# Kernel optimization log

Hardware: AMD Instinct MI355X
Metric: run time of the kernel (lower is better)

## Reference

```python
import jax, jax.numpy as jnp
import numpy as np

SUB_ARRAY_RATIO = 0.5
CENTER = False
EPS = 1e-8


def setup_inputs() -> dict:
    key = jax.random.key(0)
    X = jax.random.normal(key, (256, 8, 16384), dtype=jnp.float32)
    return {"X": X}


def reference(X) -> jnp.ndarray:
    # X: (N, M, T) real -> cast to complex64 (matches torch _ensure_complex)
    N, M, T = X.shape
    Xc = X - X.mean(axis=-1, keepdims=True) if CENTER else X
    Xc = Xc.astype(jnp.complex64)

    S = max(2, min(int(M * SUB_ARRAY_RATIO) + 1, M))  # sub_array_size
    J = M - S + 1                                      # number_of_sub_arrays

    # Full sample covariance C = X X^H / T, shape (N, M, M).
    # The per-window covariance R_j is just the SxS diagonal block of C at offset j,
    # so the forward-smoothed covariance is the mean of J shifted diagonal blocks.
    C = jnp.einsum("nmt,nkt->nmk", Xc, jnp.conj(Xc)) / T

    win = jnp.arange(J)[:, None] + jnp.arange(S)[None, :]  # (J, S) window row indices
    # Gather all J diagonal blocks: (N, J, S, S), then average over windows.
    R = C[:, win[:, :, None], win[:, None, :]].mean(axis=1)  # (N, S, S)

    rows, cols = jnp.triu_indices(S)
    tri = R[:, rows, cols]                                   # (N, S*(S+1)/2) complex
    feat = jnp.concatenate([tri.real, tri.imag], axis=1).astype(jnp.float32)

    mean = feat.mean(axis=1, keepdims=True)
    std = feat.std(axis=1, keepdims=True)  # correction=0, matches torch
    return (feat - mean) / (std + EPS)
```

## Files before the change

kernel.cpp:

```cpp
#include <hip/hip_runtime.h>
#include <math.h>

#define TLEN 16384
#define MROW 8
#define NPAIR 36
#define NTHREADS 512
#define EPSV 1e-8f

__global__ __launch_bounds__(NTHREADS)
void ssf_kernel(const float* __restrict__ X, float* __restrict__ out) {
    const int n   = blockIdx.x;
    const int tid = threadIdx.x;
    const float4* Xv = reinterpret_cast<const float4*>(X + (size_t)n * MROW * TLEN);
    const int TV = TLEN / 4;

    float acc[NPAIR];
#pragma unroll
    for (int p = 0; p < NPAIR; ++p) acc[p] = 0.f;

    for (int it = tid; it < TV; it += NTHREADS) {
        float4 x[MROW];
#pragma unroll
        for (int m = 0; m < MROW; ++m) x[m] = Xv[m * TV + it];
        const float* xv = reinterpret_cast<const float*>(x);
#pragma unroll
        for (int e = 0; e < 4; ++e) {
            int p = 0;
#pragma unroll
            for (int m = 0; m < MROW; ++m) {
                const float vm = xv[m * 4 + e];
#pragma unroll
                for (int k = m; k < MROW; ++k) {
                    acc[p++] += vm * xv[k * 4 + e];
                }
            }
        }
    }

#pragma unroll
    for (int p = 0; p < NPAIR; ++p) {
        float v = acc[p];
#pragma unroll
        for (int off = 32; off > 0; off >>= 1) v += __shfl_down(v, off, 64);
        acc[p] = v;
    }

    __shared__ float partial[NTHREADS / 64][NPAIR];
    __shared__ float Cm[MROW][MROW];
    const int wave = tid >> 6;
    const int lane = tid & 63;
    if (lane == 0) {
#pragma unroll
        for (int p = 0; p < NPAIR; ++p) partial[wave][p] = acc[p];
    }
    __syncthreads();

    if (tid < NPAIR) {
        float s = 0.f;
#pragma unroll
        for (int w = 0; w < NTHREADS / 64; ++w) s += partial[w][tid];
        s *= (1.0f / (float)TLEN);
        int p = tid, m = 0;
        while (p >= (MROW - m)) { p -= (MROW - m); ++m; }
        const int k = m + p;
        Cm[m][k] = s;
        Cm[k][m] = s;
    }
    __syncthreads();

    if (tid == 0) {
        const int rows[15] = {0,0,0,0,0, 1,1,1,1, 2,2,2, 3,3, 4};
        const int cols[15] = {0,1,2,3,4, 1,2,3,4, 2,3,4, 3,4, 4};
        float tri[15];
        float sum = 0.f;
#pragma unroll
        for (int i = 0; i < 15; ++i) {
            float r = 0.f;
#pragma unroll
            for (int j = 0; j < 4; ++j) r += Cm[j + rows[i]][j + cols[i]];
            r *= 0.25f;
            tri[i] = r;
            sum += r;
        }
        const float mean = sum * (1.0f / 30.0f);
        float var = 0.f;
#pragma unroll
        for (int i = 0; i < 15; ++i) { const float d = tri[i] - mean; var += d * d; }
        var += 15.0f * mean * mean;
        var *= (1.0f / 30.0f);
        const float inv = 1.0f / (sqrtf(var) + EPSV);

        float* o = out + (size_t)n * 30;
#pragma unroll
        for (int i = 0; i < 15; ++i) o[i] = (tri[i] - mean) * inv;
        const float zi = -mean * inv;
#pragma unroll
        for (int i = 0; i < 15; ++i) o[15 + i] = zi;
    }
}

extern "C" void kernel_launch(void* const* d_in, const int* in_sizes, int n_in,
                              void* d_out, int out_size, void* d_ws, size_t ws_size,
                              hipStream_t stream) {
    const float* X = (const float*)d_in[0];
    float* out = (float*)d_out;
    ssf_kernel<<<256, NTHREADS, 0, stream>>>(X, out);
}
```

Before: 188.4 us.

## Split time axis across blocks with two-pass reduction and prune unused pairs

Splits each sample's time axis into 8 chunks handled by separate 256-thread blocks, writing per-chunk partial covariance sums to workspace, then a second small kernel reduces them and computes features. It also only accumulates covariance entries within distance 4 of the diagonal, since only those are used by the smoothed blocks. This aims to fill the GPU with many more blocks to hide memory latency, at the cost of an extra launch and workspace traffic.

```diff
diff --git a/kernel.cpp b/kernel.cpp
--- a/kernel.cpp
+++ b/kernel.cpp
@@ -3,22 +3,29 @@
 
 #define TLEN 16384
 #define MROW 8
-#define NPAIR 36
-#define NTHREADS 512
+#define NPAIR 30
+#define NCHUNK 8
+#define NT1 256
 #define EPSV 1e-8f
 
-__global__ __launch_bounds__(NTHREADS)
-void ssf_kernel(const float* __restrict__ X, float* __restrict__ out) {
-    const int n   = blockIdx.x;
+__global__ __launch_bounds__(NT1)
+void ssf_partial(const float* __restrict__ X, float* __restrict__ part) {
+    const int b   = blockIdx.x;
+    const int n   = b >> 3;
+    const int c   = b & 7;
     const int tid = threadIdx.x;
+    const int TV  = TLEN / 4;
+    const int COLS = TV / NCHUNK;
     const float4* Xv = reinterpret_cast<const float4*>(X + (size_t)n * MROW * TLEN);
-    const int TV = TLEN / 4;
+    const int base = c * COLS;
 
     float acc[NPAIR];
 #pragma unroll
     for (int p = 0; p < NPAIR; ++p) acc[p] = 0.f;
 
-    for (int it = tid; it < TV; it += NTHREADS) {
+#pragma unroll
+    for (int i = 0; i < COLS / NT1; ++i) {
+        const int it = base + i * NT1 + tid;
         float4 x[MROW];
 #pragma unroll
         for (int m = 0; m < MROW; ++m) x[m] = Xv[m * TV + it];
@@ -29,8 +36,9 @@
 #pragma unroll
             for (int m = 0; m < MROW; ++m) {
                 const float vm = xv[m * 4 + e];
+                const int kmax = (m + 4 < MROW - 1) ? m + 4 : MROW - 1;
 #pragma unroll
-                for (int k = m; k < MROW; ++k) {
+                for (int k = m; k <= kmax; ++k) {
                     acc[p++] += vm * xv[k * 4 + e];
                 }
             }
@@ -45,8 +53,7 @@
         acc[p] = v;
     }
 
-    __shared__ float partial[NTHREADS / 64][NPAIR];
-    __shared__ float Cm[MROW][MROW];
+    __shared__ float partial[NT1 / 64][NPAIR];
     const int wave = tid >> 6;
     const int lane = tid & 63;
     if (lane == 0) {
@@ -58,10 +65,29 @@
     if (tid < NPAIR) {
         float s = 0.f;
 #pragma unroll
-        for (int w = 0; w < NTHREADS / 64; ++w) s += partial[w][tid];
+        for (int w = 0; w < NT1 / 64; ++w) s += partial[w][tid];
+        part[(size_t)b * NPAIR + tid] = s;
+    }
+}
+
+__global__ __launch_bounds__(64)
+void ssf_final(const float* __restrict__ part, float* __restrict__ out) {
+    const int n   = blockIdx.x;
+    const int tid = threadIdx.x;
+    __shared__ float Cm[MROW][MROW];
+
+    if (tid < NPAIR) {
+        float s = 0.f;
+#pragma unroll
+        for (int c = 0; c < NCHUNK; ++c)
+            s += part[((size_t)n * NCHUNK + c) * NPAIR + tid];
         s *= (1.0f / (float)TLEN);
         int p = tid, m = 0;
-        while (p >= (MROW - m)) { p -= (MROW - m); ++m; }
+        for (;;) {
+            const int cnt = ((m + 4 < MROW - 1) ? m + 4 : MROW - 1) - m + 1;
+            if (p < cnt) break;
+            p -= cnt; ++m;
+        }
         const int k = m + p;
         Cm[m][k] = s;
         Cm[k][m] = s;
@@ -103,6 +129,8 @@
                               void* d_out, int out_size, void* d_ws, size_t ws_size,
                               hipStream_t stream) {
     const float* X = (const float*)d_in[0];
-    float* out = (float*)d_out;
-    ssf_kernel<<<256, NTHREADS, 0, stream>>>(X, out);
+    float* out  = (float*)d_out;
+    float* part = (float*)d_ws;
+    ssf_partial<<<256 * NCHUNK, NT1, 0, stream>>>(X, part);
+    ssf_final<<<256, 64, 0, stream>>>(part, out);
 }
```

Result: no change. 187.8 us (-0.4%).
